# Kernel optimization log

Measured on AMD Instinct MI355X. Metric: run time of the kernel, lower is better.

The kernel has to match this reference:

```python
import jax, jax.numpy as jnp
import numpy as np

N = 512          # number of gaussians
H = 256
W = 256
TANX = 0.5
TANY = 0.5
FX = W / (2.0 * TANX)   # focal_x
FY = H / (2.0 * TANY)   # focal_y


def setup_inputs() -> dict:
    key = jax.random.key(0)
    k = jax.random.split(key, 6)
    xy = (jax.random.uniform(k[0], (N, 2)) - 0.5) * 4.0
    z = jax.random.uniform(k[1], (N, 1)) * 4.0 + 2.0   # in front of camera
    means3D = jnp.concatenate([xy, z], axis=1)
    means2D = jnp.zeros((N, 3), jnp.float32)            # gradient holder in torch; unused in math
    opacities = jax.random.uniform(k[2], (N, 1)) * 0.9 + 0.05
    colors_precomp = jax.random.uniform(k[3], (N, 3))
    scales = jax.random.uniform(k[4], (N, 3)) * 0.08 + 0.02
    rotations = jax.random.normal(k[5], (N, 4))         # normalized inside kernel, as in CUDA
    viewmatrix = jnp.eye(4, dtype=jnp.float32)
    znear, zfar = 0.01, 100.0
    proj = jnp.array([[1.0 / TANX, 0, 0, 0],
                      [0, 1.0 / TANY, 0, 0],
                      [0, 0, zfar / (zfar - znear), -(zfar * znear) / (zfar - znear)],
                      [0, 0, 1.0, 0]], dtype=jnp.float32)
    projmatrix = proj @ viewmatrix
    bg = jnp.zeros((3,), jnp.float32)
    return {"means3D": means3D, "means2D": means2D, "opacities": opacities,
            "colors_precomp": colors_precomp, "scales": scales, "rotations": rotations,
            "viewmatrix": viewmatrix, "projmatrix": projmatrix, "bg": bg}


def _forward(means3D, opacities, colors_precomp, scales, rotations, viewmatrix, projmatrix, bg):
    dt = means3D.dtype
    # --- 3D covariance from scale/rotation (computeCov3D) ---
    q = rotations / jnp.linalg.norm(rotations, axis=1, keepdims=True)
    r, x, y, z = q[:, 0], q[:, 1], q[:, 2], q[:, 3]
    R = jnp.stack([
        jnp.stack([1 - 2 * (y * y + z * z), 2 * (x * y - r * z), 2 * (x * z + r * y)], -1),
        jnp.stack([2 * (x * y + r * z), 1 - 2 * (x * x + z * z), 2 * (y * z - r * x)], -1),
        jnp.stack([2 * (x * z - r * y), 2 * (y * z + r * x), 1 - 2 * (x * x + y * y)], -1)], -2)
    Sigma = jnp.einsum('nij,nj,nkj->nik', R, scales * scales, R)   # [N,3,3]

    # --- project to camera / screen ---
    hom = jnp.concatenate([means3D, jnp.ones((means3D.shape[0], 1), dt)], 1)
    p_view = hom @ viewmatrix.T                                    # [N,4]
    tz = p_view[:, 2]
    limx, limy = 1.3 * TANX, 1.3 * TANY
    tx = jnp.clip(p_view[:, 0] / tz, -limx, limx) * tz
    ty = jnp.clip(p_view[:, 1] / tz, -limy, limy) * tz

    # --- EWA splat: cov2D = J W Sigma W^T J^T + 0.3 I ---
    zeros = jnp.zeros_like(tz)
    J = jnp.stack([jnp.stack([FX / tz, zeros, -FX * tx / (tz * tz)], -1),
                   jnp.stack([zeros, FY / tz, -FY * ty / (tz * tz)], -1)], -2)  # [N,2,3]
    Tm = jnp.einsum('nij,jk->nik', J, viewmatrix[:3, :3])
    cov2d = jnp.einsum('nij,njk,nlk->nil', Tm, Sigma, Tm)
    a = cov2d[:, 0, 0] + 0.3
    b = cov2d[:, 0, 1]
    c = cov2d[:, 1, 1] + 0.3
    det = a * c - b * b
    inv_det = 1.0 / det
    conA, conB, conC = c * inv_det, -b * inv_det, a * inv_det

    p_hom = hom @ projmatrix.T
    pw = 1.0 / (p_hom[:, 3] + 1e-7)
    pix_x = ((p_hom[:, 0] * pw + 1.0) * W - 1.0) * 0.5
    pix_y = ((p_hom[:, 1] * pw + 1.0) * H - 1.0) * 0.5

    mid = 0.5 * (a + c)
    lam = mid + jnp.sqrt(jnp.maximum(0.1, mid * mid - det))
    valid = (tz > 0.2) & (det > 0)
    radii = (jnp.ceil(3.0 * jnp.sqrt(lam)) * valid).astype(jnp.int32)

    # --- per-pixel gaussian alpha ---
    px = jnp.arange(W, dtype=dt)
    py = jnp.arange(H, dtype=dt)
    dx = pix_x[:, None, None] - px[None, None, :]   # [N,1,W]
    dy = pix_y[:, None, None] - py[None, :, None]   # [N,H,1]
    power = (-0.5 * (conA[:, None, None] * dx * dx + conC[:, None, None] * dy * dy)
             - conB[:, None, None] * dx * dy)        # [N,H,W]
    alpha = jnp.minimum(0.99, opacities[:, :, None] * jnp.exp(power))
    alpha = jnp.where((power > 0) | (alpha < 1.0 / 255.0) | (~valid[:, None, None]), 0.0, alpha)

    # --- depth sort + front-to-back alpha compositing ---
    order = jnp.argsort(tz)
    alpha_s = alpha[order]
    col_s = colors_precomp[order]
    T_inc = jnp.cumprod(1.0 - alpha_s, axis=0)                         # transmittance after each splat
    T_excl = jnp.concatenate([jnp.ones((1, H, W), dt), T_inc[:-1]], 0)  # before each splat
    wgt = alpha_s * T_excl * (T_inc >= 1e-4)                           # CUDA early-stop at T < 1e-4
    img = jnp.einsum('nhw,nc->chw', wgt, col_s) + T_inc[-1][None] * bg[:, None, None]
    return img, radii


def reference(means3D, means2D, opacities, colors_precomp, scales, rotations, viewmatrix, projmatrix, bg):
    return _forward(means3D, opacities, colors_precomp, scales, rotations, viewmatrix, projmatrix, bg)
```

## Files before the change

### kernel.cpp

```cpp
#include <hip/hip_runtime.h>
#include <hip/hip_fp16.h>
#include <math.h>

#define N_G    512
#define IMG_H  256
#define IMG_W  256

__global__ __launch_bounds__(64) void gs_prep(
    const float* __restrict__ means3D,
    const float* __restrict__ opacities,
    const float* __restrict__ colors,
    const float* __restrict__ scales,
    const float* __restrict__ rotations,
    const float* __restrict__ viewmatrix,
    const float* __restrict__ projmatrix,
    float4* __restrict__ Gs,
    float4* __restrict__ Ga,
    float2* __restrict__ Gb,
    float* __restrict__ radii_out)
{
    const int g = blockIdx.x * 64 + threadIdx.x;

    float VM[16], PM[16];
    #pragma unroll
    for (int i = 0; i < 16; ++i) { VM[i] = viewmatrix[i]; PM[i] = projmatrix[i]; }

    const float mx = means3D[g*3+0], my = means3D[g*3+1], mz = means3D[g*3+2];
    float rq = rotations[g*4+0], xq = rotations[g*4+1], yq = rotations[g*4+2], zq = rotations[g*4+3];
    const float qn = sqrtf(rq*rq + xq*xq + yq*yq + zq*zq);
    rq /= qn; xq /= qn; yq /= qn; zq /= qn;
    const float R00 = 1.f - 2.f*(yq*yq + zq*zq);
    const float R01 = 2.f*(xq*yq - rq*zq);
    const float R02 = 2.f*(xq*zq + rq*yq);
    const float R10 = 2.f*(xq*yq + rq*zq);
    const float R11 = 1.f - 2.f*(xq*xq + zq*zq);
    const float R12 = 2.f*(yq*zq - rq*xq);
    const float R20 = 2.f*(xq*zq - rq*yq);
    const float R21 = 2.f*(yq*zq + rq*xq);
    const float R22 = 1.f - 2.f*(xq*xq + yq*yq);
    float s0 = scales[g*3+0], s1 = scales[g*3+1], s2 = scales[g*3+2];
    s0 *= s0; s1 *= s1; s2 *= s2;
    const float S00 = R00*R00*s0 + R01*R01*s1 + R02*R02*s2;
    const float S01 = R00*R10*s0 + R01*R11*s1 + R02*R12*s2;
    const float S02 = R00*R20*s0 + R01*R21*s1 + R02*R22*s2;
    const float S11 = R10*R10*s0 + R11*R11*s1 + R12*R12*s2;
    const float S12 = R10*R20*s0 + R11*R21*s1 + R12*R22*s2;
    const float S22 = R20*R20*s0 + R21*R21*s1 + R22*R22*s2;

    const float pv0 = VM[0]*mx + VM[1]*my + VM[2]*mz  + VM[3];
    const float pv1 = VM[4]*mx + VM[5]*my + VM[6]*mz  + VM[7];
    const float tz  = VM[8]*mx + VM[9]*my + VM[10]*mz + VM[11];
    const float FX = 256.f, FY = 256.f, limx = 0.65f, limy = 0.65f;
    const float tx = fminf(fmaxf(pv0/tz, -limx), limx) * tz;
    const float ty = fminf(fmaxf(pv1/tz, -limy), limy) * tz;
    const float itz = 1.f / tz, itz2 = itz*itz;
    const float J00 = FX*itz, J02 = -FX*tx*itz2;
    const float J11 = FY*itz, J12 = -FY*ty*itz2;
    const float T00 = J00*VM[0] + J02*VM[8];
    const float T01 = J00*VM[1] + J02*VM[9];
    const float T02 = J00*VM[2] + J02*VM[10];
    const float T10 = J11*VM[4] + J12*VM[8];
    const float T11 = J11*VM[5] + J12*VM[9];
    const float T12 = J11*VM[6] + J12*VM[10];
    const float u0 = T00*S00 + T01*S01 + T02*S02;
    const float u1 = T00*S01 + T01*S11 + T02*S12;
    const float u2 = T00*S02 + T01*S12 + T02*S22;
    const float v0 = T10*S00 + T11*S01 + T12*S02;
    const float v1 = T10*S01 + T11*S11 + T12*S12;
    const float v2 = T10*S02 + T11*S12 + T12*S22;
    const float c00 = u0*T00 + u1*T01 + u2*T02;
    const float c01 = u0*T10 + u1*T11 + u2*T12;
    const float c11 = v0*T10 + v1*T11 + v2*T12;
    const float a = c00 + 0.3f, b = c01, c = c11 + 0.3f;
    const float det = a*c - b*b;
    const float inv_det = 1.f/det;
    float conA = c*inv_det, conB = -b*inv_det, conC = a*inv_det;
    const float ph0 = PM[0]*mx  + PM[1]*my  + PM[2]*mz  + PM[3];
    const float ph1 = PM[4]*mx  + PM[5]*my  + PM[6]*mz  + PM[7];
    const float ph3 = PM[12]*mx + PM[13]*my + PM[14]*mz + PM[15];
    const float pw = 1.f/(ph3 + 1e-7f);
    const float pix_x = ((ph0*pw + 1.f)*(float)IMG_W - 1.f)*0.5f;
    const float pix_y = ((ph1*pw + 1.f)*(float)IMG_H - 1.f)*0.5f;
    const float mid = 0.5f*(a + c);
    const float lam = mid + sqrtf(fmaxf(0.1f, mid*mid - det));
    const bool valid = (tz > 0.2f) && (det > 0.f);
    float op = opacities[g];
    if (!valid) { conA = conB = conC = 0.f; op = 0.f; }

    radii_out[g] = valid ? ceilf(3.f*sqrtf(lam)) : 0.f;

    float rad = -1.f;
    if (valid && op * 255.f > 1.f) {
        const float r = sqrtf(2.f * lam * logf(255.f * op)) + 0.01f;
        if (pix_x + r >= 0.f && pix_x - r <= (float)(IMG_W-1) &&
            pix_y + r >= 0.f && pix_y - r <= (float)(IMG_H-1))
            rad = r;
    }

    const float lnop = logf(op);
    const float rg = __builtin_bit_cast(float, __floats2half2_rn(colors[g*3+0], colors[g*3+1]));
    Gs[g] = make_float4(pix_x, pix_y, rad, tz);
    Ga[g] = make_float4(-0.5f*conA, -conB, -0.5f*conC, lnop);
    Gb[g] = make_float2(rg, colors[g*3+2]);
}

__global__ __launch_bounds__(128) void gs_raster(
    const float4* __restrict__ Gs,
    const float4* __restrict__ Ga,
    const float2* __restrict__ Gb,
    const float* __restrict__ bg,
    float* __restrict__ img)
{
    __shared__ int    s_n;
    __shared__ float  s_tz[N_G];
    __shared__ int    s_id[N_G];
    __shared__ float2 uP[N_G];
    __shared__ float4 uA[N_G];
    __shared__ float2 uC[N_G];
    __shared__ float2 oP[N_G];
    __shared__ float4 oA[N_G];
    __shared__ float2 oC[N_G];

    const int tid = threadIdx.x;
    const int bx = blockIdx.x & 15, by = blockIdx.x >> 4;
    const float x0 = (float)(bx * 16), x1 = x0 + 15.f;
    const float y0 = (float)(by * 8),  y1 = y0 + 7.f;

    if (tid == 0) s_n = 0;

    float4 s[4], a[4];
    float2 c[4];
    #pragma unroll
    for (int k = 0; k < 4; ++k) {
        const int g = k * 128 + tid;
        s[k] = Gs[g];
        a[k] = Ga[g];
        c[k] = Gb[g];
    }
    __syncthreads();

    #pragma unroll
    for (int k = 0; k < 4; ++k) {
        const bool hit = (s[k].z > 0.f &&
                          s[k].x + s[k].z >= x0 && s[k].x - s[k].z <= x1 &&
                          s[k].y + s[k].z >= y0 && s[k].y - s[k].z <= y1);
        if (hit) {
            const int p = atomicAdd(&s_n, 1);
            s_tz[p] = s[k].w;
            s_id[p] = k * 128 + tid;
            uP[p] = make_float2(s[k].x, s[k].y);
            uA[p] = a[k];
            uC[p] = c[k];
        }
    }
    __syncthreads();

    const int nc  = s_n;
    const int ncp = (nc + 7) & ~7;

    for (int i = tid; i < nc; i += 128) {
        const float tz = s_tz[i];
        const int   id = s_id[i];
        int r = 0;
        for (int j = 0; j < nc; ++j) {
            const float tj = s_tz[j];
            r += (tj < tz) || (tj == tz && s_id[j] < id);
        }
        oP[r] = uP[i];
        oA[r] = uA[i];
        oC[r] = uC[i];
    }
    for (int i = nc + tid; i < ncp; i += 128) {
        oP[i] = make_float2(0.f, 0.f);
        oA[i] = make_float4(0.f, 0.f, 0.f, -1e30f);
        oC[i] = make_float2(0.f, 0.f);
    }
    __syncthreads();

    const int px = bx * 16 + (tid & 15), py = by * 8 + (tid >> 4);
    const float fx = (float)px, fy = (float)py;

    float T = 1.f, cr = 0.f, cg = 0.f, cb = 0.f;
    bool done = false;
    for (int base = 0; base < ncp; base += 8) {
        #pragma unroll
        for (int u = 0; u < 8; ++u) {
            const int i = base + u;
            const float2 pP = oP[i];
            const float4 pA = oA[i];
            const float2 pC = oC[i];
            const float dx = pP.x - fx;
            const float dy = pP.y - fy;
            const float power = pA.x*dx*dx + pA.y*dx*dy + pA.z*dy*dy;
            const float al = fminf(0.99f, __expf(power + pA.w));
            if (!done && !(power > 0.f || al < (1.0f/255.0f))) {
                const float Tnew = T * (1.f - al);
                if (Tnew < 1e-4f) { T = Tnew; done = true; }
                else {
                    const float wgt = al * T;
                    const float2 rg = __half22float2(__builtin_bit_cast(__half2, pC.x));
                    cr += wgt * rg.x;
                    cg += wgt * rg.y;
                    cb += wgt * pC.y;
                    T = Tnew;
                }
            }
        }
        if (__all(done)) break;
    }
    const int pix = py * IMG_W + px;
    img[pix]                   = cr + T * bg[0];
    img[IMG_H*IMG_W   + pix]   = cg + T * bg[1];
    img[2*IMG_H*IMG_W + pix]   = cb + T * bg[2];
}

extern "C" void kernel_launch(void* const* d_in, const int* in_sizes, int n_in,
                              void* d_out, int out_size, void* d_ws, size_t ws_size,
                              hipStream_t stream) {
    const float* means3D    = (const float*)d_in[0];
    const float* opacities  = (const float*)d_in[2];
    const float* colors     = (const float*)d_in[3];
    const float* scales     = (const float*)d_in[4];
    const float* rotations  = (const float*)d_in[5];
    const float* viewmatrix = (const float*)d_in[6];
    const float* projmatrix = (const float*)d_in[7];
    const float* bg         = (const float*)d_in[8];

    float* img   = (float*)d_out;
    float* radii = (float*)d_out + 3*IMG_H*IMG_W;
    float4* Gs   = (float4*)d_ws;
    float4* Ga   = Gs + N_G;
    float2* Gb   = (float2*)(Ga + N_G);

    gs_prep<<<8, 64, 0, stream>>>(means3D, opacities, colors, scales,
                                  rotations, viewmatrix, projmatrix,
                                  Gs, Ga, Gb, radii);
    gs_raster<<<(IMG_W/16)*(IMG_H/8), 128, 0, stream>>>(Gs, Ga, Gb, bg, img);
}
```

Before: 19.27 us.

## Use 16x16 raster tiles, compact sort keys, and base-2 exponent in compositing

The raster tile grows from 16x8 to 16x16 pixels with 256 threads per block, which halves the number of blocks and the repeated per-block culling and sorting work. Shared staging is cut to a packed depth/id key array, and sorted Gaussian parameters are gathered from global memory by id after ranking, which lowers shared-memory use but adds scattered global loads. Conic coefficients and log-opacity are pre-scaled by log2(e) in the prep kernel so the raster loop can call the hardware exp2 directly. Larger tiles may hold more overlapping Gaussians per block and make the O(n^2) rank sort costlier, and they leave fewer blocks to spread across the GPU.

```diff
diff --git a/kernel.cpp b/kernel.cpp
--- a/kernel.cpp
+++ b/kernel.cpp
@@ -97,14 +97,15 @@
             rad = r;
     }
 
-    const float lnop = logf(op);
+    const float il2 = 1.4426950408889634f;
+    const float l2op = log2f(op);
     const float rg = __builtin_bit_cast(float, __floats2half2_rn(colors[g*3+0], colors[g*3+1]));
     Gs[g] = make_float4(pix_x, pix_y, rad, tz);
-    Ga[g] = make_float4(-0.5f*conA, -conB, -0.5f*conC, lnop);
+    Ga[g] = make_float4(-0.5f*conA*il2, -conB*il2, -0.5f*conC*il2, l2op);
     Gb[g] = make_float2(rg, colors[g*3+2]);
 }
 
-__global__ __launch_bounds__(128) void gs_raster(
+__global__ __launch_bounds__(256) void gs_raster(
     const float4* __restrict__ Gs,
     const float4* __restrict__ Ga,
     const float2* __restrict__ Gb,
@@ -112,11 +113,7 @@
     float* __restrict__ img)
 {
     __shared__ int    s_n;
-    __shared__ float  s_tz[N_G];
-    __shared__ int    s_id[N_G];
-    __shared__ float2 uP[N_G];
-    __shared__ float4 uA[N_G];
-    __shared__ float2 uC[N_G];
+    __shared__ float2 s_key[N_G];
     __shared__ float2 oP[N_G];
     __shared__ float4 oA[N_G];
     __shared__ float2 oC[N_G];
@@ -124,33 +121,23 @@
     const int tid = threadIdx.x;
     const int bx = blockIdx.x & 15, by = blockIdx.x >> 4;
     const float x0 = (float)(bx * 16), x1 = x0 + 15.f;
-    const float y0 = (float)(by * 8),  y1 = y0 + 7.f;
+    const float y0 = (float)(by * 16), y1 = y0 + 15.f;
 
     if (tid == 0) s_n = 0;
 
-    float4 s[4], a[4];
-    float2 c[4];
+    float4 s[2];
     #pragma unroll
-    for (int k = 0; k < 4; ++k) {
-        const int g = k * 128 + tid;
-        s[k] = Gs[g];
-        a[k] = Ga[g];
-        c[k] = Gb[g];
-    }
+    for (int k = 0; k < 2; ++k) s[k] = Gs[k * 256 + tid];
     __syncthreads();
 
     #pragma unroll
-    for (int k = 0; k < 4; ++k) {
+    for (int k = 0; k < 2; ++k) {
         const bool hit = (s[k].z > 0.f &&
                           s[k].x + s[k].z >= x0 && s[k].x - s[k].z <= x1 &&
                           s[k].y + s[k].z >= y0 && s[k].y - s[k].z <= y1);
         if (hit) {
             const int p = atomicAdd(&s_n, 1);
-            s_tz[p] = s[k].w;
-            s_id[p] = k * 128 + tid;
-            uP[p] = make_float2(s[k].x, s[k].y);
-            uA[p] = a[k];
-            uC[p] = c[k];
+            s_key[p] = make_float2(s[k].w, __int_as_float(k * 256 + tid));
         }
     }
     __syncthreads();
@@ -158,26 +145,28 @@
     const int nc  = s_n;
     const int ncp = (nc + 7) & ~7;
 
-    for (int i = tid; i < nc; i += 128) {
-        const float tz = s_tz[i];
-        const int   id = s_id[i];
+    for (int i = tid; i < nc; i += 256) {
+        const float2 ki = s_key[i];
+        const float tz = ki.x;
+        const int   id = __float_as_int(ki.y);
         int r = 0;
         for (int j = 0; j < nc; ++j) {
-            const float tj = s_tz[j];
-            r += (tj < tz) || (tj == tz && s_id[j] < id);
+            const float2 kj = s_key[j];
+            r += (kj.x < tz) || (kj.x == tz && __float_as_int(kj.y) < id);
         }
-        oP[r] = uP[i];
-        oA[r] = uA[i];
-        oC[r] = uC[i];
-    }
-    for (int i = nc + tid; i < ncp; i += 128) {
+        const float4 w0 = Gs[id];
+        oP[r] = make_float2(w0.x, w0.y);
+        oA[r] = Ga[id];
+        oC[r] = Gb[id];
+    }
+    for (int i = nc + tid; i < ncp; i += 256) {
         oP[i] = make_float2(0.f, 0.f);
         oA[i] = make_float4(0.f, 0.f, 0.f, -1e30f);
         oC[i] = make_float2(0.f, 0.f);
     }
     __syncthreads();
 
-    const int px = bx * 16 + (tid & 15), py = by * 8 + (tid >> 4);
+    const int px = bx * 16 + (tid & 15), py = by * 16 + (tid >> 4);
     const float fx = (float)px, fy = (float)py;
 
     float T = 1.f, cr = 0.f, cg = 0.f, cb = 0.f;
@@ -192,7 +181,7 @@
             const float dx = pP.x - fx;
             const float dy = pP.y - fy;
             const float power = pA.x*dx*dx + pA.y*dx*dy + pA.z*dy*dy;
-            const float al = fminf(0.99f, __expf(power + pA.w));
+            const float al = fminf(0.99f, __builtin_amdgcn_exp2f(power + pA.w));
             if (!done && !(power > 0.f || al < (1.0f/255.0f))) {
                 const float Tnew = T * (1.f - al);
                 if (Tnew < 1e-4f) { T = Tnew; done = true; }
@@ -235,5 +224,5 @@
     gs_prep<<<8, 64, 0, stream>>>(means3D, opacities, colors, scales,
                                   rotations, viewmatrix, projmatrix,
                                   Gs, Ga, Gb, radii);
-    gs_raster<<<(IMG_W/16)*(IMG_H/8), 128, 0, stream>>>(Gs, Ga, Gb, bg, img);
+    gs_raster<<<(IMG_W/16)*(IMG_H/16), 256, 0, stream>>>(Gs, Ga, Gb, bg, img);
 }
```

Result: faster. 18.17 us (-5.7%).
